# Kernel optimization log

Measured on AMD Instinct MI355X. Metric: run time of the kernel, lower is better.

The kernel has to match this reference:

```python
import jax, jax.numpy as jnp
import numpy as np

B, N, DIM = 8, 2048, 1024
HEADS, CB_DIM, CB_SIZE = 8, 64, 1024
CB_IN = HEADS * CB_DIM  # 512


def setup_inputs() -> dict:
    key = jax.random.key(0)
    ks = jax.random.split(key, 4)
    x = jax.random.normal(ks[0], (B, N, DIM), dtype=jnp.float32)
    W_in = jax.random.normal(ks[1], (DIM, CB_IN), dtype=jnp.float32) * (DIM ** -0.5)
    b_in = jnp.zeros((CB_IN,), dtype=jnp.float32)
    W_out = jax.random.normal(ks[2], (CB_IN, DIM), dtype=jnp.float32) * (CB_IN ** -0.5)
    b_out = jnp.zeros((DIM,), dtype=jnp.float32)
    embed = jax.random.normal(ks[3], (CB_SIZE, CB_DIM), dtype=jnp.float32)
    return {"x": x, "W_in": W_in, "b_in": b_in, "W_out": W_out, "b_out": b_out, "embed": embed}


def reference(x, W_in, b_in, W_out, b_out, embed):
    # project_in: [B, N, DIM] -> [B, N, HEADS*CB_DIM]
    h = jnp.einsum("bnd,de->bne", x, W_in) + b_in
    # multi-head split, shared codebook: 'b n (h d) -> (b h) n d' view as [B, N, H, d]
    hx = h.reshape(B, N, HEADS, CB_DIM)
    # euclidean nearest neighbor: argmin ||hx - e||^2 == argmax (2 hx.e - ||e||^2)
    dots = jnp.einsum("bnhd,cd->bnhc", hx, embed)          # [B, N, H, C]
    e_sq = jnp.sum(embed * embed, axis=-1)                    # [C]
    scores = 2.0 * dots - e_sq                                 # monotone in -dist
    embed_ind = jnp.argmax(scores, axis=-1)                    # [B, N, H] int
    quantize = embed[embed_ind]                                # [B, N, H, d] gather
    # merge heads and project_out
    q = quantize.reshape(B, N, CB_IN)
    out = jnp.einsum("bne,ed->bnd", q, W_out) + b_out          # [B, N, DIM]
    return out, embed_ind
```

## Files before the change

kernel.cpp:

```cpp
#include <hip/hip_runtime.h>

#define B_      8
#define N_      2048
#define DIM_    1024
#define HEADS_  8
#define CBD_    64
#define CBS_    1024
#define CBIN_   512
#define M_      (B_*N_)
#define M2_     (M_*HEADS_)

#define MARGIN 0.02f
#define XSTR   40

typedef unsigned short ushort_t;
typedef __attribute__((ext_vector_type(8))) short short8;
typedef __attribute__((ext_vector_type(4))) float f32x4;

__device__ inline ushort_t f2bf(float f) {
    unsigned int u = __builtin_bit_cast(unsigned int, f);
    unsigned int r = u + 0x7FFFu + ((u >> 16) & 1u);
    return (ushort_t)(r >> 16);
}
__device__ inline float bf2f(ushort_t h) {
    unsigned int u = ((unsigned int)h) << 16;
    return __builtin_bit_cast(float, u);
}
__device__ inline f32x4 mfma_bf16(short8 a, short8 b, f32x4 c) {
    return __builtin_amdgcn_mfma_f32_16x16x32_bf16(a, b, c, 0, 0, 0);
}
__device__ inline void store4u(ushort_t* p, ushort_t a, ushort_t b, ushort_t c, ushort_t d) {
    uint2 u;
    u.x = (unsigned int)a | ((unsigned int)b << 16);
    u.y = (unsigned int)c | ((unsigned int)d << 16);
    *(uint2*)p = u;
}
__device__ inline void split3(float f, ushort_t& s1, ushort_t& s2, ushort_t& s3) {
    s1 = f2bf(f);
    float r = f - bf2f(s1);
    s2 = f2bf(r);
    float r2 = r - bf2f(s2);
    s3 = f2bf(r2);
}
__device__ inline void async_cp16(void* lds, const void* g) {
    __builtin_amdgcn_global_load_lds(
        (const __attribute__((address_space(1))) unsigned int*)g,
        (__attribute__((address_space(3))) unsigned int*)lds, 16, 0, 0);
}

__global__ __launch_bounds__(256) void esq_kernel(const float* __restrict__ embed,
                                                  float* __restrict__ esq) {
    int c = blockIdx.x * 256 + threadIdx.x;
    if (c < CBS_) {
        const float* e = embed + (size_t)c * CBD_;
        float s = 0.f;
#pragma unroll
        for (int d = 0; d < CBD_; ++d) s += e[d] * e[d];
        esq[c] = s;
    }
}

__global__ __launch_bounds__(256) void split_embed(const float* __restrict__ embed,
                                                   ushort_t* __restrict__ hi,
                                                   ushort_t* __restrict__ lo) {
    int i = blockIdx.x * 256 + threadIdx.x;
    int code = i >> 6, d = i & 63;
    int dst = code * 64 + ((((d >> 3) ^ (code & 7)) << 3) | (d & 7));
    float f = embed[i];
    ushort_t hh = f2bf(f);
    hi[dst] = hh;
    lo[dst] = f2bf(f - bf2f(hh));
}

__global__ __launch_bounds__(256) void transposeW(const float* __restrict__ W,
                                                  ushort_t* __restrict__ WT) {
    __shared__ ushort_t t[64][65];
    const int tid = threadIdx.x;
    const int n0 = blockIdx.x * 64, k0 = blockIdx.y * 64;
#pragma unroll
    for (int s = 0; s < 16; ++s) {
        int i = s * 256 + tid;
        int r = i >> 6, c = i & 63;
        t[r][c] = f2bf(W[(size_t)(k0 + r) * DIM_ + n0 + c]);
    }
    __syncthreads();
#pragma unroll
    for (int s = 0; s < 16; ++s) {
        int i = s * 256 + tid;
        int r = i >> 6, c = i & 63;
        WT[(size_t)(n0 + r) * CBIN_ + k0 + c] = t[c][r];
    }
}

__global__ __launch_bounds__(256) void split_WinT(const float* __restrict__ W,
                                                  ushort_t* __restrict__ W1T,
                                                  ushort_t* __restrict__ W2T,
                                                  ushort_t* __restrict__ W3T) {
    __shared__ ushort_t t1[64][65];
    __shared__ ushort_t t2[64][65];
    __shared__ ushort_t t3[64][65];
    const int tid = threadIdx.x;
    const int n0 = blockIdx.x * 64, k0 = blockIdx.y * 64;
#pragma unroll
    for (int s = 0; s < 16; ++s) {
        int i = s * 256 + tid;
        int r = i >> 6, c = i & 63;
        float f = W[(size_t)(k0 + r) * CBIN_ + n0 + c];
        split3(f, t1[r][c], t2[r][c], t3[r][c]);
    }
    __syncthreads();
#pragma unroll
    for (int s = 0; s < 16; ++s) {
        int i = s * 256 + tid;
        int r = i >> 6, c = i & 63;
        size_t o = (size_t)(n0 + r) * DIM_ + k0 + c;
        W1T[o] = t1[c][r];
        W2T[o] = t2[c][r];
        W3T[o] = t3[c][r];
    }
}

__global__ __launch_bounds__(512) void gemm_in_x6(const float* __restrict__ x,
                                                  const ushort_t* __restrict__ W1T,
                                                  const ushort_t* __restrict__ W2T,
                                                  const ushort_t* __restrict__ W3T,
                                                  const float* __restrict__ bias,
                                                  float* __restrict__ C) {
    __shared__ ushort_t A1[128 * XSTR];
    __shared__ ushort_t A2[128 * XSTR];
    __shared__ ushort_t A3[128 * XSTR];
    __shared__ ushort_t B1[128 * XSTR];
    __shared__ ushort_t B2[128 * XSTR];
    __shared__ ushort_t B3[128 * XSTR];

    const int tid  = threadIdx.x;
    const int lane = tid & 63;
    const int w    = tid >> 6;
    const int quad = lane >> 4;
    const int col  = lane & 15;

    const int slot   = blockIdx.y * 4 + blockIdx.x;
    const int g      = slot & 7;
    const int t      = slot >> 3;
    const int m0     = (g + 8 * (t >> 2)) * 128;
    const int n0     = (t & 3) * 128;

    const int wm   = (w & 1) * 64;
    const int wn   = (w >> 1) * 32;

    f32x4 acc[4][2];
#pragma unroll
    for (int rt = 0; rt < 4; ++rt)
#pragma unroll
        for (int ct = 0; ct < 2; ++ct) acc[rt][ct] = (f32x4){0.f, 0.f, 0.f, 0.f};

    for (int k0 = 0; k0 < DIM_; k0 += 32) {
        __syncthreads();
#pragma unroll
        for (int s = 0; s < 2; ++s) {
            int f = s * 512 + tid;
            int row = f >> 3, qq = f & 7;
            float4 v = *(const float4*)(x + (size_t)(m0 + row) * DIM_ + k0 + qq * 4);
            float vv[4] = {v.x, v.y, v.z, v.w};
            ushort_t p1[4], p2[4], p3[4];
#pragma unroll
            for (int j = 0; j < 4; ++j) split3(vv[j], p1[j], p2[j], p3[j]);
            int base = row * XSTR + qq * 4;
            store4u(&A1[base], p1[0], p1[1], p1[2], p1[3]);
            store4u(&A2[base], p2[0], p2[1], p2[2], p2[3]);
            store4u(&A3[base], p3[0], p3[1], p3[2], p3[3]);
        }
        {
            int row = tid >> 2, g2 = tid & 3;
            size_t go = (size_t)(n0 + row) * DIM_ + k0 + g2 * 8;
            int lo = row * XSTR + g2 * 8;
            *(uint4*)&B1[lo] = *(const uint4*)(W1T + go);
            *(uint4*)&B2[lo] = *(const uint4*)(W2T + go);
            *(uint4*)&B3[lo] = *(const uint4*)(W3T + go);
        }
        __syncthreads();

        short8 a1[4], a2[4], a3[4], b1[2], b2[2], b3[2];
#pragma unroll
        for (int rt = 0; rt < 4; ++rt) {
            int o = (wm + rt * 16 + col) * XSTR + quad * 8;
            a1[rt] = *(const short8*)&A1[o];
            a2[rt] = *(const short8*)&A2[o];
            a3[rt] = *(const short8*)&A3[o];
        }
#pragma unroll
        for (int ct = 0; ct < 2; ++ct) {
            int o = (wn + ct * 16 + col) * XSTR + quad * 8;
            b1[ct] = *(const short8*)&B1[o];
            b2[ct] = *(const short8*)&B2[o];
            b3[ct] = *(const short8*)&B3[o];
        }
#define COMBO(AP, BP)                                                   \
        _Pragma("unroll")                                               \
        for (int ct = 0; ct < 2; ++ct)                                  \
            _Pragma("unroll")                                           \
            for (int rt = 0; rt < 4; ++rt)                              \
                acc[rt][ct] = mfma_bf16(AP[rt], BP[ct], acc[rt][ct]);
        COMBO(a1, b1); COMBO(a1, b2); COMBO(a2, b1);
        COMBO(a2, b2); COMBO(a1, b3); COMBO(a3, b1);
#undef COMBO
    }

#pragma unroll
    for (int ct = 0; ct < 2; ++ct) {
        int gc = n0 + wn + ct * 16 + col;
        float bb = bias[gc];
#pragma unroll
        for (int rt = 0; rt < 4; ++rt) {
#pragma unroll
            for (int reg = 0; reg < 4; ++reg) {
                int gr = m0 + wm + rt * 16 + quad * 4 + reg;
                C[(size_t)gr * CBIN_ + gc] = acc[rt][ct][reg] + bb;
            }
        }
    }
}

__global__ __launch_bounds__(256, 4) void argmax2(const float* __restrict__ h,
                                                  const ushort_t* __restrict__ ehswz,
                                                  const ushort_t* __restrict__ elswz,
                                                  const float* __restrict__ esq,
                                                  const float* __restrict__ embed,
                                                  float* __restrict__ outIdxF,
                                                  int* __restrict__ outIdxI) {
    __shared__ ushort_t EB[2][2][4096];
    __shared__ float    ESQ[CBS_];
    __shared__ int BIDX[128];
    __shared__ int FLAG[128];
    __shared__ int NFLAG;

    const int tid  = threadIdx.x;
    const int lane = tid & 63;
    const int w    = tid >> 6;
    const int quad = lane >> 4;
    const int col  = lane & 15;
    const int r0   = blockIdx.x * 128;

    if (tid == 0) NFLAG = 0;
    *(float4*)&ESQ[tid * 4] = *(const float4*)(esq + tid * 4);

    short8 AH[2][2], AL[2][2];
#pragma unroll
    for (int rt = 0; rt < 2; ++rt) {
        const float* hp = h + (size_t)(r0 + w * 32 + rt * 16 + col) * 64 + quad * 8;
#pragma unroll
        for (int ks = 0; ks < 2; ++ks) {
            float4 u0 = *(const float4*)(hp + ks * 32);
            float4 u1 = *(const float4*)(hp + ks * 32 + 4);
            float vv[8] = {u0.x, u0.y, u0.z, u0.w, u1.x, u1.y, u1.z, u1.w};
            short8 hh, ll;
#pragma unroll
            for (int j = 0; j < 8; ++j) {
                ushort_t hi = f2bf(vv[j]);
                hh[j] = (short)hi;
                ll[j] = (short)f2bf(vv[j] - bf2f(hi));
            }
            AH[rt][ks] = hh;
            AL[rt][ks] = ll;
        }
    }

#define STAGE(ch, b)                                                          \
    do {                                                                      \
        int eo = (ch) * 4096 + tid * 8;                                       \
        int wo = w * 512;                                                     \
        async_cp16(&EB[b][0][wo],        ehswz + eo);                         \
        async_cp16(&EB[b][0][2048 + wo], ehswz + eo + 2048);                  \
        async_cp16(&EB[b][1][wo],        elswz + eo);                         \
        async_cp16(&EB[b][1][2048 + wo], elswz + eo + 2048);                  \
    } while (0)

    STAGE(0, 0);

    float v1[8], v2[8];
    int   i1[8];
#pragma unroll
    for (int s = 0; s < 8; ++s) { v1[s] = -3.4e38f; v2[s] = -3.4e38f; i1[s] = 0; }

    __syncthreads();

    int cur = 0;
    for (int ch = 0; ch < 16; ++ch) {
        if (ch < 15) STAGE(ch + 1, cur ^ 1);
#pragma unroll
        for (int ct = 0; ct < 4; ++ct) {
            const int lc = ct * 16 + col;
            const int x7 = col & 7;
            const int o0 = lc * 64 + (((quad)     ^ x7) << 3);
            const int o1 = lc * 64 + (((quad + 4) ^ x7) << 3);
            short8 BH0 = *(const short8*)&EB[cur][0][o0];
            short8 BH1 = *(const short8*)&EB[cur][0][o1];
            short8 BL0 = *(const short8*)&EB[cur][1][o0];
            short8 BL1 = *(const short8*)&EB[cur][1][o1];
            const int code = ch * 64 + lc;
            float eq = ESQ[code];
#pragma unroll
            for (int rt = 0; rt < 2; ++rt) {
                f32x4 acc = {0.f, 0.f, 0.f, 0.f};
                acc = mfma_bf16(AH[rt][0], BH0, acc);
                acc = mfma_bf16(AH[rt][1], BH1, acc);
                acc = mfma_bf16(AH[rt][0], BL0, acc);
                acc = mfma_bf16(AH[rt][1], BL1, acc);
                acc = mfma_bf16(AL[rt][0], BH0, acc);
                acc = mfma_bf16(AL[rt][1], BH1, acc);
#pragma unroll
                for (int reg = 0; reg < 4; ++reg) {
                    const int st = rt * 4 + reg;
                    float sc = fmaf(2.f, acc[reg], -eq);
                    v2[st] = __builtin_amdgcn_fmed3f(sc, v1[st], v2[st]);
                    bool gt = sc > v1[st];
                    v1[st] = fmaxf(v1[st], sc);
                    i1[st] = gt ? code : i1[st];
                }
            }
        }
        __syncthreads();
        cur ^= 1;
    }
#undef STAGE

#pragma unroll
    for (int st = 0; st < 8; ++st) {
#pragma unroll
        for (int m = 1; m <= 8; m <<= 1) {
            float ov1 = __shfl_xor(v1[st], m);
            int   oi1 = __shfl_xor(i1[st], m);
            float ov2 = __shfl_xor(v2[st], m);
            float losr = fminf(v1[st], ov1);
            v2[st] = fmaxf(fmaxf(v2[st], ov2), losr);
            bool take = (ov1 > v1[st]) || (ov1 == v1[st] && oi1 < i1[st]);
            v1[st] = take ? ov1 : v1[st];
            i1[st] = take ? oi1 : i1[st];
        }
        if (col == 0) {
            int rt = st >> 2, reg = st & 3;
            int row_l = w * 32 + rt * 16 + quad * 4 + reg;
            BIDX[row_l] = i1[st];
            if (v1[st] - v2[st] < MARGIN) {
                int p = atomicAdd(&NFLAG, 1);
                FLAG[p] = row_l;
            }
        }
    }
    __syncthreads();

    int nf = NFLAG;
    for (int i = w; i < nf; i += 4) {
        int row_l = FLAG[i];
        const float* hr = h + (size_t)(r0 + row_l) * 64;
        float accf[16];
#pragma unroll
        for (int j = 0; j < 16; ++j) accf[j] = 0.f;
        for (int d4 = 0; d4 < 16; ++d4) {
            float4 hv = *(const float4*)(hr + d4 * 4);
#pragma unroll
            for (int j = 0; j < 16; ++j) {
                int c = lane + 64 * j;
                float4 ev = *(const float4*)(embed + (size_t)c * 64 + d4 * 4);
                accf[j] += hv.x * ev.x + hv.y * ev.y + hv.z * ev.z + hv.w * ev.w;
            }
        }
        float best = -3.4e38f; int bi = 0;
#pragma unroll
        for (int j = 0; j < 16; ++j) {
            int c = lane + 64 * j;
            float sc = 2.f * accf[j] - ESQ[c];
            if (sc > best) { best = sc; bi = c; }
        }
#pragma unroll
        for (int m = 1; m <= 32; m <<= 1) {
            float ob = __shfl_xor(best, m);
            int  obi = __shfl_xor(bi, m);
            if (ob > best || (ob == best && obi < bi)) { best = ob; bi = obi; }
        }
        if (lane == 0) BIDX[row_l] = bi;
    }
    __syncthreads();

    if (tid < 128) {
        int b = BIDX[tid];
        outIdxF[r0 + tid] = (float)b;
        outIdxI[r0 + tid] = b;
    }
}

__global__ __launch_bounds__(256) void gemm_out_bf16(const ushort_t* __restrict__ ehswz,
                                                     const int* __restrict__ idx,
                                                     const ushort_t* __restrict__ WbfT,
                                                     const float* __restrict__ bias,
                                                     float* __restrict__ C) {
    __shared__ ushort_t Qs[128 * 72];
    __shared__ ushort_t Ws[128 * 72];
    __shared__ int idxs[128 * HEADS_];

    const int tid  = threadIdx.x;
    const int lane = tid & 63;
    const int w    = tid >> 6;
    const int quad = lane >> 4;
    const int col  = lane & 15;
    const int m0   = blockIdx.y * 128;
    const int n0   = blockIdx.x * 128;
    const int wm   = (w & 1) * 64;
    const int wn   = (w >> 1) * 64;

#pragma unroll
    for (int s = 0; s < 4; ++s) {
        int f = s * 256 + tid;
        idxs[f] = idx[(size_t)m0 * HEADS_ + f];
    }

    f32x4 acc[4][4];
#pragma unroll
    for (int rt = 0; rt < 4; ++rt)
#pragma unroll
        for (int ct = 0; ct < 4; ++ct) acc[rt][ct] = (f32x4){0.f, 0.f, 0.f, 0.f};

    for (int k0 = 0; k0 < CBIN_; k0 += 64) {
        __syncthreads();
        int head = k0 >> 6;
#pragma unroll
        for (int s = 0; s < 4; ++s) {
            int f = s * 256 + tid;
            int row = f >> 3, g = f & 7;
            int e = idxs[row * HEADS_ + head];
            *(uint4*)&Qs[row * 72 + g * 8] =
                *(const uint4*)(ehswz + (size_t)e * 64 + ((g ^ (e & 7)) << 3));
            *(uint4*)&Ws[row * 72 + g * 8] =
                *(const uint4*)(WbfT + (size_t)(n0 + row) * CBIN_ + k0 + g * 8);
        }
        __syncthreads();
#pragma unroll
        for (int ks = 0; ks < 2; ++ks) {
            short8 a[4], b[4];
#pragma unroll
            for (int rt = 0; rt < 4; ++rt)
                a[rt] = *(const short8*)&Qs[(wm + rt * 16 + col) * 72 + ks * 32 + quad * 8];
#pragma unroll
            for (int ct = 0; ct < 4; ++ct)
                b[ct] = *(const short8*)&Ws[(wn + ct * 16 + col) * 72 + ks * 32 + quad * 8];
#pragma unroll
            for (int rt = 0; rt < 4; ++rt)
#pragma unroll
                for (int ct = 0; ct < 4; ++ct)
                    acc[rt][ct] = mfma_bf16(a[rt], b[ct], acc[rt][ct]);
        }
    }

#pragma unroll
    for (int ct = 0; ct < 4; ++ct) {
        int gc = n0 + wn + ct * 16 + col;
        float bb = bias[gc];
#pragma unroll
        for (int rt = 0; rt < 4; ++rt) {
#pragma unroll
            for (int reg = 0; reg < 4; ++reg) {
                int gr = m0 + wm + rt * 16 + quad * 4 + reg;
                C[(size_t)gr * DIM_ + gc] = acc[rt][ct][reg] + bb;
            }
        }
    }
}

extern "C" void kernel_launch(void* const* d_in, const int* in_sizes, int n_in,
                              void* d_out, int out_size, void* d_ws, size_t ws_size,
                              hipStream_t stream) {
    const float* x     = (const float*)d_in[0];
    const float* W_in  = (const float*)d_in[1];
    const float* b_in  = (const float*)d_in[2];
    const float* W_out = (const float*)d_in[3];
    const float* b_out = (const float*)d_in[4];
    const float* embed = (const float*)d_in[5];

    float* out     = (float*)d_out;
    float* outIdxF = out + (size_t)M_ * DIM_;

    char* ws = (char*)d_ws;
    float*    h     = (float*)ws;
    int*      idxI  = (int*)(ws + 33554432);
    float*    esq   = (float*)(ws + 34078720);
    ushort_t* ehswz = (ushort_t*)(ws + 34082816);
    ushort_t* elswz = (ushort_t*)(ws + 34213888);
    ushort_t* WbfT  = (ushort_t*)(ws + 34344960);
    ushort_t* W1T   = (ushort_t*)(ws + 35393536);
    ushort_t* W2T   = (ushort_t*)(ws + 36442112);
    ushort_t* W3T   = (ushort_t*)(ws + 37490688);

    esq_kernel<<<dim3(CBS_ / 256), dim3(256), 0, stream>>>(embed, esq);
    split_embed<<<dim3(CBS_ * CBD_ / 256), dim3(256), 0, stream>>>(embed, ehswz, elswz);
    transposeW<<<dim3(DIM_ / 64, CBIN_ / 64), dim3(256), 0, stream>>>(W_out, WbfT);
    split_WinT<<<dim3(CBIN_ / 64, DIM_ / 64), dim3(256), 0, stream>>>(W_in, W1T, W2T, W3T);
    gemm_in_x6<<<dim3(CBIN_ / 128, M_ / 128), dim3(512), 0, stream>>>(x, W1T, W2T, W3T,
                                                                      b_in, h);
    argmax2<<<dim3(M2_ / 128), dim3(256), 0, stream>>>(h, ehswz, elswz, esq, embed,
                                                       outIdxF, idxI);
    gemm_out_bf16<<<dim3(DIM_ / 128, M_ / 128), dim3(256), 0, stream>>>(ehswz, idxI, WbfT,
                                                                        b_out, out);
}
```

Before: 365.4 us.

## Replace gathered output GEMM with per-head codebook projection table plus gather-sum

```diff
diff --git a/kernel.cpp b/kernel.cpp
--- a/kernel.cpp
+++ b/kernel.cpp
@@ -389,30 +389,33 @@
     }
 }
 
-__global__ __launch_bounds__(256) void gemm_out_bf16(const ushort_t* __restrict__ ehswz,
-                                                     const int* __restrict__ idx,
-                                                     const ushort_t* __restrict__ WbfT,
-                                                     const float* __restrict__ bias,
-                                                     float* __restrict__ C) {
-    __shared__ ushort_t Qs[128 * 72];
+__global__ __launch_bounds__(256) void computeP(const ushort_t* __restrict__ ehswz,
+                                                const ushort_t* __restrict__ WbfT,
+                                                float* __restrict__ P) {
+    __shared__ ushort_t Es[128 * 72];
     __shared__ ushort_t Ws[128 * 72];
-    __shared__ int idxs[128 * HEADS_];
 
     const int tid  = threadIdx.x;
     const int lane = tid & 63;
     const int w    = tid >> 6;
     const int quad = lane >> 4;
     const int col  = lane & 15;
-    const int m0   = blockIdx.y * 128;
     const int n0   = blockIdx.x * 128;
+    const int c0   = blockIdx.y * 128;
+    const int hh   = blockIdx.z;
     const int wm   = (w & 1) * 64;
     const int wn   = (w >> 1) * 64;
 
 #pragma unroll
     for (int s = 0; s < 4; ++s) {
         int f = s * 256 + tid;
-        idxs[f] = idx[(size_t)m0 * HEADS_ + f];
-    }
+        int row = f >> 3, g = f & 7;
+        *(uint4*)&Es[row * 72 + g * 8] =
+            *(const uint4*)(ehswz + (size_t)(c0 + row) * 64 + ((g ^ (row & 7)) << 3));
+        *(uint4*)&Ws[row * 72 + g * 8] =
+            *(const uint4*)(WbfT + (size_t)(n0 + row) * CBIN_ + hh * 64 + g * 8);
+    }
+    __syncthreads();
 
     f32x4 acc[4][4];
 #pragma unroll
@@ -420,49 +423,59 @@
 #pragma unroll
         for (int ct = 0; ct < 4; ++ct) acc[rt][ct] = (f32x4){0.f, 0.f, 0.f, 0.f};
 
-    for (int k0 = 0; k0 < CBIN_; k0 += 64) {
-        __syncthreads();
-        int head = k0 >> 6;
-#pragma unroll
-        for (int s = 0; s < 4; ++s) {
-            int f = s * 256 + tid;
-            int row = f >> 3, g = f & 7;
-            int e = idxs[row * HEADS_ + head];
-            *(uint4*)&Qs[row * 72 + g * 8] =
-                *(const uint4*)(ehswz + (size_t)e * 64 + ((g ^ (e & 7)) << 3));
-            *(uint4*)&Ws[row * 72 + g * 8] =
-                *(const uint4*)(WbfT + (size_t)(n0 + row) * CBIN_ + k0 + g * 8);
-        }
-        __syncthreads();
-#pragma unroll
-        for (int ks = 0; ks < 2; ++ks) {
-            short8 a[4], b[4];
-#pragma unroll
-            for (int rt = 0; rt < 4; ++rt)
-                a[rt] = *(const short8*)&Qs[(wm + rt * 16 + col) * 72 + ks * 32 + quad * 8];
+#pragma unroll
+    for (int ks = 0; ks < 2; ++ks) {
+        short8 a[4], b[4];
+#pragma unroll
+        for (int rt = 0; rt < 4; ++rt)
+            a[rt] = *(const short8*)&Es[(wm + rt * 16 + col) * 72 + ks * 32 + quad * 8];
+#pragma unroll
+        for (int ct = 0; ct < 4; ++ct)
+            b[ct] = *(const short8*)&Ws[(wn + ct * 16 + col) * 72 + ks * 32 + quad * 8];
+#pragma unroll
+        for (int rt = 0; rt < 4; ++rt)
 #pragma unroll
             for (int ct = 0; ct < 4; ++ct)
-                b[ct] = *(const short8*)&Ws[(wn + ct * 16 + col) * 72 + ks * 32 + quad * 8];
-#pragma unroll
-            for (int rt = 0; rt < 4; ++rt)
-#pragma unroll
-                for (int ct = 0; ct < 4; ++ct)
-                    acc[rt][ct] = mfma_bf16(a[rt], b[ct], acc[rt][ct]);
-        }
+                acc[rt][ct] = mfma_bf16(a[rt], b[ct], acc[rt][ct]);
     }
 
 #pragma unroll
     for (int ct = 0; ct < 4; ++ct) {
-        int gc = n0 + wn + ct * 16 + col;
-        float bb = bias[gc];
+        int gn = n0 + wn + ct * 16 + col;
 #pragma unroll
         for (int rt = 0; rt < 4; ++rt) {
 #pragma unroll
             for (int reg = 0; reg < 4; ++reg) {
-                int gr = m0 + wm + rt * 16 + quad * 4 + reg;
-                C[(size_t)gr * DIM_ + gc] = acc[rt][ct][reg] + bb;
+                int gc = c0 + wm + rt * 16 + quad * 4 + reg;
+                P[((size_t)hh * CBS_ + gc) * DIM_ + gn] = acc[rt][ct][reg];
             }
         }
+    }
+}
+
+__global__ __launch_bounds__(256) void gather_out(const float* __restrict__ P,
+                                                  const int* __restrict__ idx,
+                                                  const float* __restrict__ b_out,
+                                                  float* __restrict__ out) {
+    __shared__ int ids[16 * HEADS_];
+    const int tid = threadIdx.x;
+    const int r0  = blockIdx.x * 16;
+
+    if (tid < 16 * HEADS_) ids[tid] = idx[(size_t)r0 * HEADS_ + tid];
+    __syncthreads();
+
+    const float4 bb = *(const float4*)(b_out + tid * 4);
+#pragma unroll 2
+    for (int r = 0; r < 16; ++r) {
+        float4 acc = bb;
+#pragma unroll
+        for (int hh = 0; hh < 8; ++hh) {
+            int e = ids[r * HEADS_ + hh];
+            const float4 pv =
+                *(const float4*)(P + ((size_t)hh * CBS_ + e) * DIM_ + tid * 4);
+            acc.x += pv.x; acc.y += pv.y; acc.z += pv.z; acc.w += pv.w;
+        }
+        *(float4*)(out + (size_t)(r0 + r) * DIM_ + tid * 4) = acc;
     }
 }
 
@@ -481,6 +494,7 @@
 
     char* ws = (char*)d_ws;
     float*    h     = (float*)ws;
+    float*    P     = (float*)ws;
     int*      idxI  = (int*)(ws + 33554432);
     float*    esq   = (float*)(ws + 34078720);
     ushort_t* ehswz = (ushort_t*)(ws + 34082816);
@@ -498,6 +512,6 @@
                                                                       b_in, h);
     argmax2<<<dim3(M2_ / 128), dim3(256), 0, stream>>>(h, ehswz, elswz, esq, embed,
                                                        outIdxF, idxI);
-    gemm_out_bf16<<<dim3(DIM_ / 128, M_ / 128), dim3(256), 0, stream>>>(ehswz, idxI, WbfT,
-                                                                        b_out, out);
-}
+    computeP<<<dim3(DIM_ / 128, CBS_ / 128, HEADS_), dim3(256), 0, stream>>>(ehswz, WbfT, P);
+    gather_out<<<dim3(M_ / 16), dim3(256), 0, stream>>>(P, idxI, b_out, out);
+}
```

Result: slower. 392.8 us (+7.5%).

## Triple-buffer codebook chunks in argmax kernel with partial vmcnt waits

Applied to the files above, without the earlier changes.

```diff
diff --git a/kernel.cpp b/kernel.cpp
--- a/kernel.cpp
+++ b/kernel.cpp
@@ -228,7 +228,7 @@
                                                   const float* __restrict__ embed,
                                                   float* __restrict__ outIdxF,
                                                   int* __restrict__ outIdxI) {
-    __shared__ ushort_t EB[2][2][4096];
+    __shared__ ushort_t EB[3 * 2 * 4096];
     __shared__ float    ESQ[CBS_];
     __shared__ int BIDX[128];
     __shared__ int FLAG[128];
@@ -268,14 +268,15 @@
 #define STAGE(ch, b)                                                          \
     do {                                                                      \
         int eo = (ch) * 4096 + tid * 8;                                       \
-        int wo = w * 512;                                                     \
-        async_cp16(&EB[b][0][wo],        ehswz + eo);                         \
-        async_cp16(&EB[b][0][2048 + wo], ehswz + eo + 2048);                  \
-        async_cp16(&EB[b][1][wo],        elswz + eo);                         \
-        async_cp16(&EB[b][1][2048 + wo], elswz + eo + 2048);                  \
+        int dz = (b) * 8192 + w * 512;                                        \
+        async_cp16(&EB[dz],        ehswz + eo);                               \
+        async_cp16(&EB[dz + 2048], ehswz + eo + 2048);                        \
+        async_cp16(&EB[dz + 4096],        elswz + eo);                        \
+        async_cp16(&EB[dz + 4096 + 2048], elswz + eo + 2048);                 \
     } while (0)
 
     STAGE(0, 0);
+    STAGE(1, 1);
 
     float v1[8], v2[8];
     int   i1[8];
@@ -285,18 +286,20 @@
     __syncthreads();
 
     int cur = 0;
+#pragma unroll
     for (int ch = 0; ch < 16; ++ch) {
-        if (ch < 15) STAGE(ch + 1, cur ^ 1);
+        if (ch < 14) STAGE(ch + 2, (cur == 0) ? 2 : cur - 1);
+        const int bz = cur * 8192;
 #pragma unroll
         for (int ct = 0; ct < 4; ++ct) {
             const int lc = ct * 16 + col;
             const int x7 = col & 7;
             const int o0 = lc * 64 + (((quad)     ^ x7) << 3);
             const int o1 = lc * 64 + (((quad + 4) ^ x7) << 3);
-            short8 BH0 = *(const short8*)&EB[cur][0][o0];
-            short8 BH1 = *(const short8*)&EB[cur][0][o1];
-            short8 BL0 = *(const short8*)&EB[cur][1][o0];
-            short8 BL1 = *(const short8*)&EB[cur][1][o1];
+            short8 BH0 = *(const short8*)&EB[bz + o0];
+            short8 BH1 = *(const short8*)&EB[bz + o1];
+            short8 BL0 = *(const short8*)&EB[bz + 4096 + o0];
+            short8 BL1 = *(const short8*)&EB[bz + 4096 + o1];
             const int code = ch * 64 + lc;
             float eq = ESQ[code];
 #pragma unroll
@@ -319,8 +322,13 @@
                 }
             }
         }
-        __syncthreads();
-        cur ^= 1;
+        if (ch < 15) {
+            if (ch < 14) asm volatile("s_waitcnt vmcnt(4)" ::: "memory");
+            else         asm volatile("s_waitcnt vmcnt(0)" ::: "memory");
+            __builtin_amdgcn_s_barrier();
+            __builtin_amdgcn_sched_barrier(0);
+        }
+        cur = (cur == 2) ? 0 : cur + 1;
     }
 #undef STAGE
 
```

New measurement: 738.4 us. +102.1%, slower.
